# Kernel tuning notes

Measured on AMD Instinct MI355X. Metric: run time of the kernel, lower is better.

The kernel has to match this reference:

```python
import jax, jax.numpy as jnp
import numpy as np

DIM = 1024

def setup_inputs() -> dict:
    key = jax.random.key(0)
    ks = jax.random.split(key, 7)
    s = 1.0 / np.sqrt(DIM)  # roughly match nn.Linear init scale
    return {
        "x": jax.random.normal(ks[0], (4, 2048, DIM), dtype=jnp.float32),
        "Wq": jax.random.normal(ks[1], (DIM, DIM), dtype=jnp.float32) * s,
        "bq": jax.random.normal(ks[2], (DIM,), dtype=jnp.float32) * s,
        "Wk": jax.random.normal(ks[3], (DIM, DIM), dtype=jnp.float32) * s,
        "bk": jax.random.normal(ks[4], (DIM,), dtype=jnp.float32) * s,
        "Wv": jax.random.normal(ks[5], (DIM, DIM), dtype=jnp.float32) * s,
        "bv": jax.random.normal(ks[6], (DIM,), dtype=jnp.float32) * s,
    }

def reference(x, Wq, bq, Wk, bk, Wv, bv):
    # torch Linear: y = x @ W.T + b
    C = x.shape[-1]
    scale = C ** (-0.5)
    q = jnp.einsum('bnc,dc->bnd', x, Wq) + bq
    k = jnp.einsum('bnc,dc->bnd', x, Wk) + bk
    v = jnp.einsum('bnc,dc->bnd', x, Wv) + bv
    attn = jnp.einsum('bnd,bmd->bnm', q, k) * scale  # [B,N,N]
    attn = jax.nn.softmax(attn, axis=-1)
    out = jnp.einsum('bnm,bmd->bnd', attn, v)
    return out
```

## Files before the change

### kernel.cpp

```cpp
#include <hip/hip_runtime.h>

#define SEQ  2048
#define DIM  1024
#define NTOK 8192
#define NQKV 3072
#define BK   64

typedef __attribute__((ext_vector_type(8)))  __bf16 bf16x8;
typedef __attribute__((ext_vector_type(16))) float  f32x16;

__device__ __forceinline__ unsigned short f2bf(float f) {
    unsigned int u = __float_as_uint(f);
    u += 0x7fffu + ((u >> 16) & 1u);
    return (unsigned short)(u >> 16);
}

__device__ __forceinline__ float bfu2f(unsigned int lo16) {
    return __uint_as_float(lo16 << 16);
}

__device__ __forceinline__ void load_lds_128(const unsigned short* g, unsigned short* l) {
    __builtin_amdgcn_global_load_lds(
        (const __attribute__((address_space(1))) void*)g,
        (__attribute__((address_space(3))) void*)l, 16, 0, 0);
}

template <int MODE>
__global__ __launch_bounds__(256)
void gemm_bt(const unsigned short* __restrict__ A, const unsigned short* __restrict__ B,
             void* __restrict__ Cv,
             const float* __restrict__ b0, const float* __restrict__ b1,
             const float* __restrict__ b2, unsigned short* __restrict__ vt,
             const float* __restrict__ inv_rs,
             int K, int lda, int ldb, int ldc,
             long sA, long sB, long sC, float alpha)
{
    __shared__ unsigned short As[128 * BK];
    __shared__ unsigned short Bs[128 * BK];

    const int tid  = threadIdx.x;
    const int wave = tid >> 6;
    const int lane = tid & 63;
    const int l31  = lane & 31;
    const int half = lane >> 5;

    const int m0 = blockIdx.x * 128;
    const int n0 = blockIdx.y * 128;
    const int z  = blockIdx.z;
    A += (long)z * sA;
    B += (long)z * sB;

    const int wm = (wave >> 1) * 64;
    const int wn = (wave & 1) * 64;

    f32x16 acc[2][2] = {};

    const int r0 = tid >> 3;
    const int g  = ((tid & 7) - r0) & 7;
    const unsigned short* Ag = A + (long)(m0 + r0) * lda + g * 8;
    const unsigned short* Bg = B + (long)(n0 + r0) * ldb + g * 8;
    unsigned short* Al = As + tid * 8;
    unsigned short* Bl = Bs + tid * 8;

    const unsigned short* Af[2][4];
    const unsigned short* Bf[2][4];
#pragma unroll
    for (int i = 0; i < 2; ++i) {
        const int rrA = wm + i * 32 + l31;
        const int rrB = wn + i * 32 + l31;
#pragma unroll
        for (int h = 0; h < 4; ++h) {
            const int gw = h * 2 + half;
            Af[i][h] = As + rrA * BK + (((gw + rrA) & 7) << 3);
            Bf[i][h] = Bs + rrB * BK + (((gw + rrB) & 7) << 3);
        }
    }

    for (int k0 = 0; k0 < K; k0 += BK) {
#pragma unroll
        for (int p = 0; p < 4; ++p) {
            load_lds_128(Ag + k0 + (long)(32 * p) * lda, Al + 2048 * p);
            load_lds_128(Bg + k0 + (long)(32 * p) * ldb, Bl + 2048 * p);
        }
        __syncthreads();
        bf16x8 a[2][4], b[2][4];
#pragma unroll
        for (int i = 0; i < 2; ++i)
#pragma unroll
            for (int h = 0; h < 4; ++h) {
                a[i][h] = *(const bf16x8*)Af[i][h];
                b[i][h] = *(const bf16x8*)Bf[i][h];
            }
#pragma unroll
        for (int h = 0; h < 4; ++h)
#pragma unroll
            for (int i = 0; i < 2; ++i)
#pragma unroll
                for (int j = 0; j < 2; ++j)
                    acc[i][j] = __builtin_amdgcn_mfma_f32_32x32x16_bf16(
                        a[i][h], b[j][h], acc[i][j], 0, 0, 0);
        __syncthreads();
    }

    if (MODE == 0) {
        if (n0 >= 2048) {
#pragma unroll
            for (int j = 0; j < 2; ++j) {
                const int d = n0 - 2048 + wn + j * 32 + l31;
                const float bias = b2[d];
#pragma unroll
                for (int i = 0; i < 2; ++i) {
                    const int mbase = m0 + wm + i * 32 + 4 * half;
#pragma unroll
                    for (int rq = 0; rq < 4; ++rq) {
                        const int rowi = mbase + 8 * rq;
                        const int bb = rowi >> 11;
                        const int mm = rowi & 2047;
                        ushort4 u;
                        u.x = f2bf(acc[i][j][rq * 4 + 0] + bias);
                        u.y = f2bf(acc[i][j][rq * 4 + 1] + bias);
                        u.z = f2bf(acc[i][j][rq * 4 + 2] + bias);
                        u.w = f2bf(acc[i][j][rq * 4 + 3] + bias);
                        *(ushort4*)(vt + ((long)bb * DIM + d) * SEQ + mm) = u;
                    }
                }
            }
        } else {
            unsigned short* C16 = (unsigned short*)Cv;
#pragma unroll
            for (int j = 0; j < 2; ++j) {
                const int col = n0 + wn + j * 32 + l31;
                const float* bp = (col >> 10) ? b1 : b0;
                const float bias = bp[col & 1023];
#pragma unroll
                for (int i = 0; i < 2; ++i)
#pragma unroll
                    for (int r = 0; r < 16; ++r) {
                        const int rowi = m0 + wm + i * 32 + (r & 3) + 8 * (r >> 2) + 4 * half;
                        C16[(long)rowi * ldc + col] = f2bf(acc[i][j][r] + bias);
                    }
            }
        }
    } else if (MODE == 1) {
        float* C = (float*)Cv + (long)z * sC;
        const float* ir = inv_rs + (long)z * SEQ;
#pragma unroll
        for (int i = 0; i < 2; ++i) {
            const int rbase = m0 + wm + i * 32 + 4 * half;
#pragma unroll
            for (int rq = 0; rq < 4; ++rq) {
                const float4 inv4 = *(const float4*)(ir + rbase + 8 * rq);
#pragma unroll
                for (int j = 0; j < 2; ++j) {
                    const int col = n0 + wn + j * 32 + l31;
                    C[(long)(rbase + 8 * rq + 0) * ldc + col] = acc[i][j][rq * 4 + 0] * inv4.x;
                    C[(long)(rbase + 8 * rq + 1) * ldc + col] = acc[i][j][rq * 4 + 1] * inv4.y;
                    C[(long)(rbase + 8 * rq + 2) * ldc + col] = acc[i][j][rq * 4 + 2] * inv4.z;
                    C[(long)(rbase + 8 * rq + 3) * ldc + col] = acc[i][j][rq * 4 + 3] * inv4.w;
                }
            }
        }
    } else {
        unsigned short* C16 = (unsigned short*)Cv + (long)z * sC;
#pragma unroll
        for (int j = 0; j < 2; ++j) {
            const int col = n0 + wn + j * 32 + l31;
#pragma unroll
            for (int i = 0; i < 2; ++i)
#pragma unroll
                for (int r = 0; r < 16; ++r) {
                    const int rowi = m0 + wm + i * 32 + (r & 3) + 8 * (r >> 2) + 4 * half;
                    C16[(long)rowi * ldc + col] = f2bf(__expf(acc[i][j][r] * alpha));
                }
        }
    }
}

__global__ __launch_bounds__(256)
void cvt_x(const float* __restrict__ src, unsigned short* __restrict__ dst, int n4)
{
    int i = blockIdx.x * 256 + threadIdx.x;
    if (i < n4) {
        float4 f = ((const float4*)src)[i];
        ushort4 u;
        u.x = f2bf(f.x); u.y = f2bf(f.y); u.z = f2bf(f.z); u.w = f2bf(f.w);
        ((ushort4*)dst)[i] = u;
    }
}

__global__ __launch_bounds__(256)
void cvt_w3(const float* __restrict__ Wq, const float* __restrict__ Wk,
            const float* __restrict__ Wv, unsigned short* __restrict__ dst)
{
    const int sel = blockIdx.y;
    const float* src = (sel == 0) ? Wq : ((sel == 1) ? Wk : Wv);
    const int i = blockIdx.x * 256 + threadIdx.x;
    float4 f = ((const float4*)src)[i];
    ushort4 u;
    u.x = f2bf(f.x); u.y = f2bf(f.y); u.z = f2bf(f.z); u.w = f2bf(f.w);
    ((ushort4*)(dst + (long)sel * DIM * DIM))[i] = u;
}

__global__ __launch_bounds__(256)
void rowsum_inv(const unsigned short* __restrict__ P, float* __restrict__ inv_rs)
{
    const int row  = blockIdx.x * 4 + (threadIdx.x >> 6);
    const int lane = threadIdx.x & 63;
    const unsigned short* pr = P + (long)row * SEQ;

    float s = 0.f;
#pragma unroll
    for (int it = 0; it < 4; ++it) {
        uint4 u = *(const uint4*)(pr + (it * 64 + lane) * 8);
        s += bfu2f(u.x & 0xffffu) + __uint_as_float(u.x & 0xffff0000u);
        s += bfu2f(u.y & 0xffffu) + __uint_as_float(u.y & 0xffff0000u);
        s += bfu2f(u.z & 0xffffu) + __uint_as_float(u.z & 0xffff0000u);
        s += bfu2f(u.w & 0xffffu) + __uint_as_float(u.w & 0xffff0000u);
    }
    for (int off = 32; off > 0; off >>= 1)
        s += __shfl_xor(s, off);
    if (lane == 0) inv_rs[row] = 1.0f / s;
}

extern "C" void kernel_launch(void* const* d_in, const int* in_sizes, int n_in,
                              void* d_out, int out_size, void* d_ws, size_t ws_size,
                              hipStream_t stream)
{
    const float* x  = (const float*)d_in[0];
    const float* Wq = (const float*)d_in[1];
    const float* bq = (const float*)d_in[2];
    const float* Wk = (const float*)d_in[3];
    const float* bk = (const float*)d_in[4];
    const float* Wv = (const float*)d_in[5];
    const float* bv = (const float*)d_in[6];
    float* out = (float*)d_out;

    char* ws = (char*)d_ws;
    unsigned short* xb   = (unsigned short*)ws;
    unsigned short* Wb   = (unsigned short*)(ws + 16u * 1024 * 1024);
    unsigned short* qkv  = (unsigned short*)(ws + 64u * 1024 * 1024);
    unsigned short* vt   = (unsigned short*)(ws + 112u * 1024 * 1024);
    unsigned short* P    = (unsigned short*)(ws + 128u * 1024 * 1024);
    float*          irs  = (float*)(ws + 160u * 1024 * 1024);

    const float scale = 0.03125f;
    dim3 blk(256);

    cvt_x<<<NTOK * DIM / 4 / 256, blk, 0, stream>>>(x, xb, NTOK * DIM / 4);
    cvt_w3<<<dim3(DIM * DIM / 4 / 256, 3), blk, 0, stream>>>(Wq, Wk, Wv, Wb);

    gemm_bt<0><<<dim3(NTOK / 128, NQKV / 128), blk, 0, stream>>>(
        xb, Wb, qkv, bq, bk, bv, vt, nullptr,
        DIM, DIM, DIM, NQKV, 0, 0, 0, 1.0f);

    gemm_bt<2><<<dim3(SEQ / 128, SEQ / 128, 4), blk, 0, stream>>>(
        qkv, qkv + 1024, P, nullptr, nullptr, nullptr, nullptr, nullptr,
        DIM, NQKV, NQKV, SEQ,
        (long)SEQ * NQKV, (long)SEQ * NQKV, (long)SEQ * SEQ, scale);

    rowsum_inv<<<NTOK / 4, blk, 0, stream>>>(P, irs);

    gemm_bt<1><<<dim3(SEQ / 128, DIM / 128, 4), blk, 0, stream>>>(
        P, vt, out, nullptr, nullptr, nullptr, nullptr, irs,
        SEQ, SEQ, SEQ, DIM,
        (long)SEQ * SEQ, (long)DIM * SEQ, (long)SEQ * DIM, 1.0f);
}
```

Before: 268.3 us.

## Rewrite GEMMs as 256-row tiles with 4-stage LDS pipelining and 16x16 MFMA

Replaces the 128x128 single-buffered GEMM with a 512-thread kernel using 256-row tiles (256x128 or 256x256), a 4-deep ring of LDS buffers fed by async global-to-LDS loads three steps ahead, and 16x16x32 MFMA instructions. Explicit waitcnt, barriers, sched_barrier and setprio interleave loads with MFMA work to hide memory latency and raise arithmetic intensity. The LDS swizzle is dropped, so bank conflicts on fragment reads may appear. Larger tiles also reduce grid size and occupancy for the smaller GEMMs.

```diff
diff --git a/kernel.cpp b/kernel.cpp
--- a/kernel.cpp
+++ b/kernel.cpp
@@ -4,10 +4,9 @@
 #define DIM  1024
 #define NTOK 8192
 #define NQKV 3072
-#define BK   64
-
-typedef __attribute__((ext_vector_type(8)))  __bf16 bf16x8;
-typedef __attribute__((ext_vector_type(16))) float  f32x16;
+
+typedef __attribute__((ext_vector_type(8))) __bf16 bf16x8;
+typedef __attribute__((ext_vector_type(4))) float  f32x4;
 
 __device__ __forceinline__ unsigned short f2bf(float f) {
     unsigned int u = __float_as_uint(f);
@@ -25,9 +24,9 @@
         (__attribute__((address_space(3))) void*)l, 16, 0, 0);
 }
 
-template <int MODE>
-__global__ __launch_bounds__(256)
-void gemm_bt(const unsigned short* __restrict__ A, const unsigned short* __restrict__ B,
+template <int MODE, int NF>
+__global__ __launch_bounds__(512, 2)
+void gemm256(const unsigned short* __restrict__ A, const unsigned short* __restrict__ B,
              void* __restrict__ Cv,
              const float* __restrict__ b0, const float* __restrict__ b1,
              const float* __restrict__ b2, unsigned short* __restrict__ vt,
@@ -35,143 +34,187 @@
              int K, int lda, int ldb, int ldc,
              long sA, long sB, long sC, float alpha)
 {
-    __shared__ unsigned short As[128 * BK];
-    __shared__ unsigned short Bs[128 * BK];
+    constexpr int BN  = NF * 64;
+    constexpr int AT  = 256 * 32;
+    constexpr int BT  = BN * 32;
+    constexpr int LPT = 2 + BN / 128;
+
+    __shared__ unsigned short As[4 * AT];
+    __shared__ unsigned short Bs[4 * BT];
 
     const int tid  = threadIdx.x;
     const int wave = tid >> 6;
     const int lane = tid & 63;
-    const int l31  = lane & 31;
-    const int half = lane >> 5;
-
-    const int m0 = blockIdx.x * 128;
-    const int n0 = blockIdx.y * 128;
+    const int l4   = lane & 15;
+    const int lh   = lane >> 4;
+    const int wm   = wave >> 2;
+    const int wn   = wave & 3;
+
+    const int m0 = blockIdx.x * 256;
+    const int n0 = blockIdx.y * BN;
     const int z  = blockIdx.z;
     A += (long)z * sA;
     B += (long)z * sB;
 
-    const int wm = (wave >> 1) * 64;
-    const int wn = (wave & 1) * 64;
-
-    f32x16 acc[2][2] = {};
-
-    const int r0 = tid >> 3;
-    const int g  = ((tid & 7) - r0) & 7;
-    const unsigned short* Ag = A + (long)(m0 + r0) * lda + g * 8;
-    const unsigned short* Bg = B + (long)(n0 + r0) * ldb + g * 8;
-    unsigned short* Al = As + tid * 8;
-    unsigned short* Bl = Bs + tid * 8;
-
-    const unsigned short* Af[2][4];
-    const unsigned short* Bf[2][4];
-#pragma unroll
-    for (int i = 0; i < 2; ++i) {
-        const int rrA = wm + i * 32 + l31;
-        const int rrB = wn + i * 32 + l31;
-#pragma unroll
-        for (int h = 0; h < 4; ++h) {
-            const int gw = h * 2 + half;
-            Af[i][h] = As + rrA * BK + (((gw + rrA) & 7) << 3);
-            Bf[i][h] = Bs + rrB * BK + (((gw + rrB) & 7) << 3);
+    const unsigned short* Ag0 = A + (long)(m0 + (tid >> 2)) * lda + (tid & 3) * 8;
+    const unsigned short* Ag1 = Ag0 + (long)128 * lda;
+    const unsigned short* Bg0 = B + (long)(n0 + (tid >> 2)) * ldb + (tid & 3) * 8;
+    const unsigned short* Bg1 = Bg0 + (long)128 * ldb;
+    unsigned short* Al0 = As + tid * 8;
+    unsigned short* Bl0 = Bs + tid * 8;
+
+    const int NT = K >> 5;
+
+    auto stageA = [&](int t) {
+        const int bo = (t & 3) * AT;
+        load_lds_128(Ag0 + (long)t * 32, Al0 + bo);
+        load_lds_128(Ag1 + (long)t * 32, Al0 + bo + 4096);
+    };
+    auto stageB = [&](int t) {
+        const int bo = (t & 3) * BT;
+        load_lds_128(Bg0 + (long)t * 32, Bl0 + bo);
+        if constexpr (NF == 4)
+            load_lds_128(Bg1 + (long)t * 32, Bl0 + bo + 4096);
+    };
+
+    const int aoff = (wm * 128 + l4) * 32 + lh * 8;
+    const int boff = (wn * (BN / 4) + l4) * 32 + lh * 8;
+
+    f32x4 acc[8][NF] = {};
+
+    stageA(0); stageB(0);
+    stageA(1); stageB(1);
+    stageA(2); stageB(2);
+    asm volatile("s_waitcnt vmcnt(%0)" :: "n"(2 * LPT) : "memory");
+    __builtin_amdgcn_s_barrier();
+
+    for (int t = 0; t < NT; ++t) {
+        const int bi = t & 3;
+        const unsigned short* Ab = As + bi * AT + aoff;
+        const unsigned short* Bb = Bs + bi * BT + boff;
+        bf16x8 b[NF];
+
+        if constexpr (NF == 4) {
+            bf16x8 a[4];
+#pragma unroll
+            for (int nf = 0; nf < 4; ++nf) b[nf] = *(const bf16x8*)(Bb + nf * 512);
+#pragma unroll
+            for (int mf = 0; mf < 4; ++mf) a[mf] = *(const bf16x8*)(Ab + mf * 512);
+            if (t + 3 < NT) stageA(t + 3);
+            __builtin_amdgcn_s_barrier();
+            asm volatile("s_waitcnt lgkmcnt(0)" ::: "memory");
+            __builtin_amdgcn_sched_barrier(0);
+            __builtin_amdgcn_s_setprio(1);
+#pragma unroll
+            for (int mf = 0; mf < 4; ++mf)
+#pragma unroll
+                for (int nf = 0; nf < 4; ++nf)
+                    acc[mf][nf] = __builtin_amdgcn_mfma_f32_16x16x32_bf16(
+                        a[mf], b[nf], acc[mf][nf], 0, 0, 0);
+            __builtin_amdgcn_s_setprio(0);
+            __builtin_amdgcn_s_barrier();
+#pragma unroll
+            for (int mf = 0; mf < 4; ++mf) a[mf] = *(const bf16x8*)(Ab + (mf + 4) * 512);
+            if (t + 3 < NT) stageB(t + 3);
+            __builtin_amdgcn_s_barrier();
+            asm volatile("s_waitcnt lgkmcnt(0)" ::: "memory");
+            __builtin_amdgcn_sched_barrier(0);
+            __builtin_amdgcn_s_setprio(1);
+#pragma unroll
+            for (int mf = 0; mf < 4; ++mf)
+#pragma unroll
+                for (int nf = 0; nf < 4; ++nf)
+                    acc[mf + 4][nf] = __builtin_amdgcn_mfma_f32_16x16x32_bf16(
+                        a[mf], b[nf], acc[mf + 4][nf], 0, 0, 0);
+            __builtin_amdgcn_s_setprio(0);
+            asm volatile("s_waitcnt vmcnt(%0)" :: "n"(2 * LPT) : "memory");
+            __builtin_amdgcn_s_barrier();
+        } else {
+            bf16x8 a8[8];
+#pragma unroll
+            for (int nf = 0; nf < NF; ++nf) b[nf] = *(const bf16x8*)(Bb + nf * 512);
+#pragma unroll
+            for (int mf = 0; mf < 8; ++mf) a8[mf] = *(const bf16x8*)(Ab + mf * 512);
+            if (t + 3 < NT) { stageA(t + 3); stageB(t + 3); }
+            __builtin_amdgcn_s_barrier();
+            asm volatile("s_waitcnt lgkmcnt(0)" ::: "memory");
+            __builtin_amdgcn_sched_barrier(0);
+            __builtin_amdgcn_s_setprio(1);
+#pragma unroll
+            for (int mf = 0; mf < 8; ++mf)
+#pragma unroll
+                for (int nf = 0; nf < NF; ++nf)
+                    acc[mf][nf] = __builtin_amdgcn_mfma_f32_16x16x32_bf16(
+                        a8[mf], b[nf], acc[mf][nf], 0, 0, 0);
+            __builtin_amdgcn_s_setprio(0);
+            asm volatile("s_waitcnt vmcnt(%0)" :: "n"(2 * LPT) : "memory");
+            __builtin_amdgcn_s_barrier();
         }
     }
 
-    for (int k0 = 0; k0 < K; k0 += BK) {
-#pragma unroll
-        for (int p = 0; p < 4; ++p) {
-            load_lds_128(Ag + k0 + (long)(32 * p) * lda, Al + 2048 * p);
-            load_lds_128(Bg + k0 + (long)(32 * p) * ldb, Bl + 2048 * p);
-        }
-        __syncthreads();
-        bf16x8 a[2][4], b[2][4];
-#pragma unroll
-        for (int i = 0; i < 2; ++i)
-#pragma unroll
-            for (int h = 0; h < 4; ++h) {
-                a[i][h] = *(const bf16x8*)Af[i][h];
-                b[i][h] = *(const bf16x8*)Bf[i][h];
-            }
-#pragma unroll
-        for (int h = 0; h < 4; ++h)
-#pragma unroll
-            for (int i = 0; i < 2; ++i)
-#pragma unroll
-                for (int j = 0; j < 2; ++j)
-                    acc[i][j] = __builtin_amdgcn_mfma_f32_32x32x16_bf16(
-                        a[i][h], b[j][h], acc[i][j], 0, 0, 0);
-        __syncthreads();
-    }
+    const int r0 = m0 + wm * 128 + lh * 4;
+    const int c0 = n0 + wn * (BN / 4) + l4;
 
     if (MODE == 0) {
         if (n0 >= 2048) {
 #pragma unroll
-            for (int j = 0; j < 2; ++j) {
-                const int d = n0 - 2048 + wn + j * 32 + l31;
+            for (int nf = 0; nf < NF; ++nf) {
+                const int d = c0 + nf * 16 - 2048;
                 const float bias = b2[d];
 #pragma unroll
-                for (int i = 0; i < 2; ++i) {
-                    const int mbase = m0 + wm + i * 32 + 4 * half;
-#pragma unroll
-                    for (int rq = 0; rq < 4; ++rq) {
-                        const int rowi = mbase + 8 * rq;
-                        const int bb = rowi >> 11;
-                        const int mm = rowi & 2047;
-                        ushort4 u;
-                        u.x = f2bf(acc[i][j][rq * 4 + 0] + bias);
-                        u.y = f2bf(acc[i][j][rq * 4 + 1] + bias);
-                        u.z = f2bf(acc[i][j][rq * 4 + 2] + bias);
-                        u.w = f2bf(acc[i][j][rq * 4 + 3] + bias);
-                        *(ushort4*)(vt + ((long)bb * DIM + d) * SEQ + mm) = u;
-                    }
+                for (int mf = 0; mf < 8; ++mf) {
+                    const int row = r0 + mf * 16;
+                    const int bb = row >> 11;
+                    const int mm = row & 2047;
+                    ushort4 u;
+                    u.x = f2bf(acc[mf][nf][0] + bias);
+                    u.y = f2bf(acc[mf][nf][1] + bias);
+                    u.z = f2bf(acc[mf][nf][2] + bias);
+                    u.w = f2bf(acc[mf][nf][3] + bias);
+                    *(ushort4*)(vt + ((long)bb * DIM + d) * SEQ + mm) = u;
                 }
             }
         } else {
             unsigned short* C16 = (unsigned short*)Cv;
 #pragma unroll
-            for (int j = 0; j < 2; ++j) {
-                const int col = n0 + wn + j * 32 + l31;
-                const float* bp = (col >> 10) ? b1 : b0;
-                const float bias = bp[col & 1023];
-#pragma unroll
-                for (int i = 0; i < 2; ++i)
-#pragma unroll
-                    for (int r = 0; r < 16; ++r) {
-                        const int rowi = m0 + wm + i * 32 + (r & 3) + 8 * (r >> 2) + 4 * half;
-                        C16[(long)rowi * ldc + col] = f2bf(acc[i][j][r] + bias);
-                    }
+            for (int nf = 0; nf < NF; ++nf) {
+                const int col = c0 + nf * 16;
+                const float bias = (col >= 1024) ? b1[col - 1024] : b0[col];
+#pragma unroll
+                for (int mf = 0; mf < 8; ++mf)
+#pragma unroll
+                    for (int r = 0; r < 4; ++r)
+                        C16[(long)(r0 + mf * 16 + r) * ldc + col] =
+                            f2bf(acc[mf][nf][r] + bias);
             }
         }
     } else if (MODE == 1) {
         float* C = (float*)Cv + (long)z * sC;
         const float* ir = inv_rs + (long)z * SEQ;
 #pragma unroll
-        for (int i = 0; i < 2; ++i) {
-            const int rbase = m0 + wm + i * 32 + 4 * half;
-#pragma unroll
-            for (int rq = 0; rq < 4; ++rq) {
-                const float4 inv4 = *(const float4*)(ir + rbase + 8 * rq);
-#pragma unroll
-                for (int j = 0; j < 2; ++j) {
-                    const int col = n0 + wn + j * 32 + l31;
-                    C[(long)(rbase + 8 * rq + 0) * ldc + col] = acc[i][j][rq * 4 + 0] * inv4.x;
-                    C[(long)(rbase + 8 * rq + 1) * ldc + col] = acc[i][j][rq * 4 + 1] * inv4.y;
-                    C[(long)(rbase + 8 * rq + 2) * ldc + col] = acc[i][j][rq * 4 + 2] * inv4.z;
-                    C[(long)(rbase + 8 * rq + 3) * ldc + col] = acc[i][j][rq * 4 + 3] * inv4.w;
-                }
+        for (int mf = 0; mf < 8; ++mf) {
+            const int row = r0 + mf * 16;
+            const float4 inv4 = *(const float4*)(ir + row);
+#pragma unroll
+            for (int nf = 0; nf < NF; ++nf) {
+                const int col = c0 + nf * 16;
+                C[(long)(row + 0) * ldc + col] = acc[mf][nf][0] * inv4.x;
+                C[(long)(row + 1) * ldc + col] = acc[mf][nf][1] * inv4.y;
+                C[(long)(row + 2) * ldc + col] = acc[mf][nf][2] * inv4.z;
+                C[(long)(row + 3) * ldc + col] = acc[mf][nf][3] * inv4.w;
             }
         }
     } else {
         unsigned short* C16 = (unsigned short*)Cv + (long)z * sC;
 #pragma unroll
-        for (int j = 0; j < 2; ++j) {
-            const int col = n0 + wn + j * 32 + l31;
-#pragma unroll
-            for (int i = 0; i < 2; ++i)
-#pragma unroll
-                for (int r = 0; r < 16; ++r) {
-                    const int rowi = m0 + wm + i * 32 + (r & 3) + 8 * (r >> 2) + 4 * half;
-                    C16[(long)rowi * ldc + col] = f2bf(__expf(acc[i][j][r] * alpha));
-                }
+        for (int nf = 0; nf < NF; ++nf) {
+            const int col = c0 + nf * 16;
+#pragma unroll
+            for (int mf = 0; mf < 8; ++mf)
+#pragma unroll
+                for (int r = 0; r < 4; ++r)
+                    C16[(long)(r0 + mf * 16 + r) * ldc + col] =
+                        f2bf(__expf(acc[mf][nf][r] * alpha));
         }
     }
 }
@@ -245,22 +288,23 @@
 
     const float scale = 0.03125f;
     dim3 blk(256);
+    dim3 blk512(512);
 
     cvt_x<<<NTOK * DIM / 4 / 256, blk, 0, stream>>>(x, xb, NTOK * DIM / 4);
     cvt_w3<<<dim3(DIM * DIM / 4 / 256, 3), blk, 0, stream>>>(Wq, Wk, Wv, Wb);
 
-    gemm_bt<0><<<dim3(NTOK / 128, NQKV / 128), blk, 0, stream>>>(
+    gemm256<0, 2><<<dim3(NTOK / 256, NQKV / 128), blk512, 0, stream>>>(
         xb, Wb, qkv, bq, bk, bv, vt, nullptr,
         DIM, DIM, DIM, NQKV, 0, 0, 0, 1.0f);
 
-    gemm_bt<2><<<dim3(SEQ / 128, SEQ / 128, 4), blk, 0, stream>>>(
+    gemm256<2, 4><<<dim3(SEQ / 256, SEQ / 256, 4), blk512, 0, stream>>>(
         qkv, qkv + 1024, P, nullptr, nullptr, nullptr, nullptr, nullptr,
         DIM, NQKV, NQKV, SEQ,
         (long)SEQ * NQKV, (long)SEQ * NQKV, (long)SEQ * SEQ, scale);
 
     rowsum_inv<<<NTOK / 4, blk, 0, stream>>>(P, irs);
 
-    gemm_bt<1><<<dim3(SEQ / 128, DIM / 128, 4), blk, 0, stream>>>(
+    gemm256<1, 2><<<dim3(SEQ / 256, DIM / 128, 4), blk512, 0, stream>>>(
         P, vt, out, nullptr, nullptr, nullptr, nullptr, irs,
         SEQ, SEQ, SEQ, DIM,
         (long)SEQ * SEQ, (long)DIM * SEQ, (long)SEQ * DIM, 1.0f);
```

New measurement: 274.2 us. 2.2% more time.
